# Kernel tuning notes

Measured on AMD Instinct MI355X. Metric: run time of the kernel, lower is better.

Reference implementation:

```python
import jax, jax.numpy as jnp
import numpy as np

N_NODES = 50000
N_EDGES = 800000
D = 64
E_DIM = 16
N_GRAPHS = 5000
BN_EPS = 1e-5


def _xavier(key, shape):
    fan_in, fan_out = shape[0], shape[1]
    limit = np.sqrt(6.0 / (fan_in + fan_out))
    return jax.random.uniform(key, shape, jnp.float32, -limit, limit)


def setup_inputs() -> dict:
    key = jax.random.key(0)
    ks = jax.random.split(key, 16)
    x = jax.random.normal(ks[0], (N_NODES, D), jnp.float32)
    edge_index = jax.random.randint(ks[1], (2, N_EDGES), 0, N_NODES, jnp.int64)
    edge_attr = jax.random.normal(ks[2], (N_EDGES, E_DIM), jnp.float32)
    batch = jnp.sort(jax.random.randint(ks[3], (N_NODES,), 0, N_GRAPHS, jnp.int64))
    zdim = 2 * D + E_DIM  # 144
    params = {
        'fw0': _xavier(ks[4], (zdim, D)), 'fb0': jnp.zeros((D,), jnp.float32),
        'sw0': _xavier(ks[5], (zdim, D)), 'sb0': jnp.zeros((D,), jnp.float32),
        'bng0': jnp.ones((D,), jnp.float32), 'bnb0': jnp.zeros((D,), jnp.float32),
        'fw1': _xavier(ks[6], (zdim, D)), 'fb1': jnp.zeros((D,), jnp.float32),
        'sw1': _xavier(ks[7], (zdim, D)), 'sb1': jnp.zeros((D,), jnp.float32),
        'bng1': jnp.ones((D,), jnp.float32), 'bnb1': jnp.zeros((D,), jnp.float32),
        'pw1': _xavier(ks[8], (D, D)), 'pb1': jnp.zeros((D,), jnp.float32),
        'pw2': _xavier(ks[9], (D, D)), 'pb2': jnp.zeros((D,), jnp.float32),
    }
    return dict(x=x, edge_index=edge_index, edge_attr=edge_attr, batch=batch, **params)


def _cgconv(x, src, dst, e, Wf, bf, Ws, bs):
    # PyG CGConv: x_i' = x_i + sum_j sigmoid(Wf z) * softplus(Ws z), z=[x_i, x_j, e]
    # edge_index[0]=source j, edge_index[1]=target i; aggregate at target.
    z = jnp.concatenate([x[dst], x[src], e], axis=-1)  # [E, 2D+Ed]
    m = jax.nn.sigmoid(z @ Wf + bf) * jax.nn.softplus(z @ Ws + bs)  # [E, D]
    agg = jax.ops.segment_sum(m, dst, num_segments=x.shape[0])
    return x + agg


def _batchnorm(x, gamma, beta):
    mu = jnp.mean(x, axis=0)
    var = jnp.mean(jnp.square(x - mu), axis=0)  # biased, training-mode BN
    return (x - mu) * jax.lax.rsqrt(var + BN_EPS) * gamma + beta


def reference(x, edge_index, edge_attr, batch,
              fw0, fb0, sw0, sb0, bng0, bnb0,
              fw1, fb1, sw1, sb1, bng1, bnb1,
              pw1, pb1, pw2, pb2):
    src, dst = edge_index[0], edge_index[1]
    h = _batchnorm(_cgconv(x, src, dst, edge_attr, fw0, fb0, sw0, sb0), bng0, bnb0)
    h = _batchnorm(_cgconv(h, src, dst, edge_attr, fw1, fb1, sw1, sb1), bng1, bnb1)
    # global mean pool over graphs
    sums = jax.ops.segment_sum(h, batch, num_segments=N_GRAPHS)
    cnt = jax.ops.segment_sum(jnp.ones((h.shape[0],), h.dtype), batch, num_segments=N_GRAPHS)
    pooled = sums / jnp.maximum(cnt, 1.0)[:, None]  # [G, D]
    # proj head: Linear -> LeakyReLU(0.01) -> Linear
    y = jax.nn.leaky_relu(pooled @ pw1 + pb1, negative_slope=0.01)
    return y @ pw2 + pb2
```

## Files before the change

### kernel.cpp

```cpp
#include <hip/hip_runtime.h>

#define NN 50000
#define NE 800000
#define DD 64
#define ED 16
#define NG 5000
#define SS 16

__global__ __launch_bounds__(256) void prep_weights(
    const float* __restrict__ fw0, const float* __restrict__ sw0,
    const float* __restrict__ fw1, const float* __restrict__ sw1,
    float2* __restrict__ Wd0, float2* __restrict__ Wsc0, float2* __restrict__ We0,
    float2* __restrict__ Wd1, float2* __restrict__ Wsc1, float2* __restrict__ We1) {
  int i = blockIdx.x * 256 + threadIdx.x;
  if (i >= 2 * 144 * 64) return;
  int layer = i >= 144 * 64;
  int j = i - layer * 144 * 64;
  int k = j >> 6, d = j & 63;
  const float* fw = layer ? fw1 : fw0;
  const float* sw = layer ? sw1 : sw0;
  float2 v = make_float2(fw[j], sw[j]);
  float2* Wd = layer ? Wd1 : Wd0;
  float2* Wsc = layer ? Wsc1 : Wsc0;
  float2* We = layer ? We1 : We0;
  if (k < 64)       Wd[k * DD + d] = v;
  else if (k < 128) Wsc[(k - 64) * DD + d] = v;
  else              We[(k - 128) * DD + d] = v;
}

__global__ __launch_bounds__(256) void k_hist(const int* __restrict__ ei,
                                              int* __restrict__ deg) {
  int e = blockIdx.x * 256 + threadIdx.x;
  if (e < NE) atomicAdd(&deg[ei[NE + e]], 1);
}

__global__ __launch_bounds__(256) void k_scan1(const int* __restrict__ deg,
                                               int* __restrict__ rowptr,
                                               int* __restrict__ partials) {
  __shared__ int sm[256];
  int t = threadIdx.x, i = blockIdx.x * 256 + t;
  int v = (i < NN) ? deg[i] : 0;
  sm[t] = v; __syncthreads();
  for (int off = 1; off < 256; off <<= 1) {
    int x = (t >= off) ? sm[t - off] : 0;
    __syncthreads();
    sm[t] += x;
    __syncthreads();
  }
  if (i < NN) rowptr[i] = sm[t] - v;
  if (t == 255) partials[blockIdx.x] = sm[255];
}

__global__ __launch_bounds__(256) void k_scan2(int* __restrict__ partials,
                                               int* __restrict__ poff, int nparts) {
  __shared__ int sm[256];
  int t = threadIdx.x;
  int v = (t < nparts) ? partials[t] : 0;
  sm[t] = v; __syncthreads();
  for (int off = 1; off < 256; off <<= 1) {
    int x = (t >= off) ? sm[t - off] : 0;
    __syncthreads();
    sm[t] += x;
    __syncthreads();
  }
  poff[t] = sm[t] - v;
}

__global__ __launch_bounds__(256) void k_scan3(int* __restrict__ rowptr,
                                               int* __restrict__ cursor,
                                               const int* __restrict__ poff) {
  int i = blockIdx.x * 256 + threadIdx.x;
  if (i < NN) {
    int v = rowptr[i] + poff[blockIdx.x];
    rowptr[i] = v;
    cursor[i] = v;
  } else if (i == NN) {
    rowptr[NN] = NE;
  }
}

__global__ __launch_bounds__(256) void k_scatter(const int* __restrict__ ei,
                                                 const float4* __restrict__ ea4,
                                                 int* __restrict__ cursor,
                                                 int* __restrict__ ssrc,
                                                 int* __restrict__ sdst,
                                                 float4* __restrict__ sea4) {
  int e = blockIdx.x * 256 + threadIdx.x;
  if (e >= NE) return;
  int dst = ei[NE + e];
  int pos = atomicAdd(&cursor[dst], 1);
  ssrc[pos] = ei[e];
  sdst[pos] = dst;
  const float4* q = ea4 + (size_t)e * 4;
  float4 a0 = q[0], a1 = q[1], a2 = q[2], a3 = q[3];
  float4* o = sea4 + (size_t)pos * 4;
  o[0] = a0; o[1] = a1; o[2] = a2; o[3] = a3;
}

template <int BN>
__global__ __launch_bounds__(256) void node_transform(
    const float* __restrict__ hin, const float* __restrict__ stats,
    const float* __restrict__ gamma, const float* __restrict__ beta,
    const float2* __restrict__ Wd, const float2* __restrict__ Wsc,
    const float* __restrict__ bf, const float* __restrict__ sbv,
    float2* __restrict__ Dst, float2* __restrict__ Src,
    float* __restrict__ hcopy) {
  __shared__ float hrow[32][DD];
  int tid = threadIdx.x, w = tid >> 6, d = tid & 63;
  int nbase = blockIdx.x * 32;
  const float invN = 1.f / (float)NN;
#pragma unroll
  for (int j = 0; j < 2; ++j) {
    int i4 = tid + j * 256;
    int node = nbase + (i4 >> 4);
    if (node < NN) {
      int c = (i4 & 15) * 4;
      float4 v = *(const float4*)(hin + (size_t)node * DD + c);
      if (BN) {
        float mu0 = stats[c + 0] * invN, va0 = stats[64 + c + 0] * invN - mu0 * mu0;
        float mu1 = stats[c + 1] * invN, va1 = stats[64 + c + 1] * invN - mu1 * mu1;
        float mu2 = stats[c + 2] * invN, va2 = stats[64 + c + 2] * invN - mu2 * mu2;
        float mu3 = stats[c + 3] * invN, va3 = stats[64 + c + 3] * invN - mu3 * mu3;
        float sc0 = rsqrtf(va0 + 1e-5f) * gamma[c + 0];
        float sc1 = rsqrtf(va1 + 1e-5f) * gamma[c + 1];
        float sc2 = rsqrtf(va2 + 1e-5f) * gamma[c + 2];
        float sc3 = rsqrtf(va3 + 1e-5f) * gamma[c + 3];
        v.x = fmaf(v.x, sc0, beta[c + 0] - mu0 * sc0);
        v.y = fmaf(v.y, sc1, beta[c + 1] - mu1 * sc1);
        v.z = fmaf(v.z, sc2, beta[c + 2] - mu2 * sc2);
        v.w = fmaf(v.w, sc3, beta[c + 3] - mu3 * sc3);
      }
      *(float4*)(&hrow[i4 >> 4][c]) = v;
      *(float4*)(hcopy + (size_t)node * DD + c) = v;
    }
  }
  __syncthreads();

  float bfd = bf[d], sbd = sbv[d];
  float2 ad[8], as_[8];
#pragma unroll
  for (int i = 0; i < 8; ++i) { ad[i] = make_float2(bfd, sbd); as_[i] = make_float2(0.f, 0.f); }

  for (int kk = 0; kk < 16; ++kk) {
    int k0 = kk * 4;
    float2 wd0 = Wd[(k0 + 0) * DD + d], wd1 = Wd[(k0 + 1) * DD + d];
    float2 wd2 = Wd[(k0 + 2) * DD + d], wd3 = Wd[(k0 + 3) * DD + d];
    float2 ws0 = Wsc[(k0 + 0) * DD + d], ws1 = Wsc[(k0 + 1) * DD + d];
    float2 ws2 = Wsc[(k0 + 2) * DD + d], ws3 = Wsc[(k0 + 3) * DD + d];
#pragma unroll
    for (int i = 0; i < 8; ++i) {
      float4 hv = *(const float4*)(&hrow[w * 8 + i][k0]);
      ad[i].x = fmaf(hv.x, wd0.x, ad[i].x); ad[i].y = fmaf(hv.x, wd0.y, ad[i].y);
      as_[i].x = fmaf(hv.x, ws0.x, as_[i].x); as_[i].y = fmaf(hv.x, ws0.y, as_[i].y);
      ad[i].x = fmaf(hv.y, wd1.x, ad[i].x); ad[i].y = fmaf(hv.y, wd1.y, ad[i].y);
      as_[i].x = fmaf(hv.y, ws1.x, as_[i].x); as_[i].y = fmaf(hv.y, ws1.y, as_[i].y);
      ad[i].x = fmaf(hv.z, wd2.x, ad[i].x); ad[i].y = fmaf(hv.z, wd2.y, ad[i].y);
      as_[i].x = fmaf(hv.z, ws2.x, as_[i].x); as_[i].y = fmaf(hv.z, ws2.y, as_[i].y);
      ad[i].x = fmaf(hv.w, wd3.x, ad[i].x); ad[i].y = fmaf(hv.w, wd3.y, ad[i].y);
      as_[i].x = fmaf(hv.w, ws3.x, as_[i].x); as_[i].y = fmaf(hv.w, ws3.y, as_[i].y);
    }
  }
#pragma unroll
  for (int i = 0; i < 8; ++i) {
    int n = nbase + w * 8 + i;
    if (n < NN) {
      Dst[(size_t)n * DD + d] = ad[i];
      Src[(size_t)n * DD + d] = as_[i];
    }
  }
}

__global__ __launch_bounds__(256, 4) void conv_strip(
    const int* __restrict__ ssrc, const int* __restrict__ sdst,
    const float4* __restrict__ sea4, const float2* __restrict__ We,
    const float2* __restrict__ Dst, const float2* __restrict__ Src,
    float* __restrict__ out) {
  __shared__ float4 sEA[4][SS * 4];
  __shared__ int sid[4][2 * SS];
  int tid = threadIdx.x, w = tid >> 6, d = tid & 63;
  int strip = blockIdx.x * 4 + w;
  size_t base = (size_t)strip * SS;

  sEA[w][d] = sea4[base * 4 + d];
  if (d < 2 * SS) sid[w][d] = (d < SS) ? ssrc[base + d] : sdst[base + d - SS];
  __syncthreads();

  float2 we[16];
#pragma unroll
  for (int k = 0; k < 16; ++k) we[k] = We[k * DD + d];

  float2 b[SS];
#pragma unroll
  for (int i = 0; i < SS; ++i) b[i] = Src[(size_t)sid[w][i] * DD + d];

  int curdst = sid[w][SS];
  float2 a = Dst[(size_t)curdst * DD + d];
  float acc = 0.f;
#pragma unroll
  for (int i = 0; i < SS; ++i) {
    int dstn = sid[w][SS + i];
    if (dstn != curdst) {
      atomicAdd(&out[(size_t)curdst * DD + d], acc);
      acc = 0.f;
      curdst = dstn;
      a = Dst[(size_t)curdst * DD + d];
    }
    float cf = a.x + b[i].x, cs = a.y + b[i].y;
#pragma unroll
    for (int k = 0; k < 4; ++k) {
      float4 z = sEA[w][i * 4 + k];
      cf = fmaf(z.x, we[4 * k + 0].x, cf); cs = fmaf(z.x, we[4 * k + 0].y, cs);
      cf = fmaf(z.y, we[4 * k + 1].x, cf); cs = fmaf(z.y, we[4 * k + 1].y, cs);
      cf = fmaf(z.z, we[4 * k + 2].x, cf); cs = fmaf(z.z, we[4 * k + 2].y, cs);
      cf = fmaf(z.w, we[4 * k + 3].x, cf); cs = fmaf(z.w, we[4 * k + 3].y, cs);
    }
    float sig = __builtin_amdgcn_rcpf(1.f + __expf(-cf));
    float sp  = fmaxf(cs, 0.f) + __logf(1.f + __expf(-fabsf(cs)));
    acc = fmaf(sig, sp, acc);
  }
  atomicAdd(&out[(size_t)curdst * DD + d], acc);
}

__global__ __launch_bounds__(256) void bn_stats(const float* __restrict__ h,
                                                float* __restrict__ stats) {
  int tid = threadIdx.x;
  int c = (tid & 15) * 4;
  int r0 = blockIdx.x * 16 + (tid >> 4);
  float4 s = make_float4(0, 0, 0, 0), ss = make_float4(0, 0, 0, 0);
  for (int r = r0; r < NN; r += gridDim.x * 16) {
    float4 v = *(const float4*)(h + (size_t)r * DD + c);
    s.x += v.x; s.y += v.y; s.z += v.z; s.w += v.w;
    ss.x += v.x * v.x; ss.y += v.y * v.y; ss.z += v.z * v.z; ss.w += v.w * v.w;
  }
  __shared__ float4 sm[256], sm2[256];
  sm[tid] = s; sm2[tid] = ss;
  __syncthreads();
  for (int str = 128; str >= 16; str >>= 1) {
    if (tid < str) {
      sm[tid].x += sm[tid + str].x; sm[tid].y += sm[tid + str].y;
      sm[tid].z += sm[tid + str].z; sm[tid].w += sm[tid + str].w;
      sm2[tid].x += sm2[tid + str].x; sm2[tid].y += sm2[tid + str].y;
      sm2[tid].z += sm2[tid + str].z; sm2[tid].w += sm2[tid + str].w;
    }
    __syncthreads();
  }
  if (tid < 16) {
    int cc = tid * 4;
    atomicAdd(&stats[cc + 0], sm[tid].x); atomicAdd(&stats[cc + 1], sm[tid].y);
    atomicAdd(&stats[cc + 2], sm[tid].z); atomicAdd(&stats[cc + 3], sm[tid].w);
    atomicAdd(&stats[64 + cc + 0], sm2[tid].x); atomicAdd(&stats[64 + cc + 1], sm2[tid].y);
    atomicAdd(&stats[64 + cc + 2], sm2[tid].z); atomicAdd(&stats[64 + cc + 3], sm2[tid].w);
  }
}

__global__ __launch_bounds__(256) void pool_bn(
    const float* __restrict__ h, const int* __restrict__ batch,
    const float* __restrict__ stats,
    const float* __restrict__ gamma, const float* __restrict__ beta,
    float* __restrict__ psum, float* __restrict__ pcnt) {
  int tid = threadIdx.x, g = tid >> 6, d = tid & 63;
  const float invN = 1.f / (float)NN;
  float mu = stats[d] * invN;
  float var = stats[64 + d] * invN - mu * mu;
  float sc = rsqrtf(var + 1e-5f) * gamma[d];
  float sh = beta[d] - mu * sc;
  int n0 = (blockIdx.x * 4 + g) * 32;
  if (n0 >= NN) return;
  int nend = n0 + 32; if (nend > NN) nend = NN;
  int bprev = batch[n0];
  float acc = 0.f; int run = 0;
  for (int n = n0; n < nend; ++n) {
    int b = batch[n];
    if (b != bprev) {
      atomicAdd(&psum[(size_t)bprev * DD + d], acc);
      if (d == 0) atomicAdd(&pcnt[bprev], (float)run);
      acc = 0.f; run = 0; bprev = b;
    }
    acc += fmaf(h[(size_t)n * DD + d], sc, sh);
    ++run;
  }
  atomicAdd(&psum[(size_t)bprev * DD + d], acc);
  if (d == 0) atomicAdd(&pcnt[bprev], (float)run);
}

__global__ __launch_bounds__(256) void head_kernel(
    const float* __restrict__ psum, const float* __restrict__ pcnt,
    const float* __restrict__ pw1, const float* __restrict__ pb1,
    const float* __restrict__ pw2, const float* __restrict__ pb2,
    float* __restrict__ out) {
  __shared__ float row[4][DD], y1[4][DD];
  int tid = threadIdx.x, g = tid >> 6, d = tid & 63;
  int q = blockIdx.x * 4 + g;
  float c = fmaxf(pcnt[q], 1.0f);
  row[g][d] = psum[(size_t)q * DD + d] * __builtin_amdgcn_rcpf(c);
  __syncthreads();
  float acc = pb1[d];
#pragma unroll
  for (int k = 0; k < DD; ++k) acc = fmaf(row[g][k], pw1[k * DD + d], acc);
  acc = acc > 0.f ? acc : 0.01f * acc;
  y1[g][d] = acc;
  __syncthreads();
  float o = pb2[d];
#pragma unroll
  for (int k = 0; k < DD; ++k) o = fmaf(y1[g][k], pw2[k * DD + d], o);
  out[(size_t)q * DD + d] = o;
}

extern "C" void kernel_launch(void* const* d_in, const int* in_sizes, int n_in,
                              void* d_out, int out_size, void* d_ws, size_t ws_size,
                              hipStream_t stream) {
  const float* x     = (const float*)d_in[0];
  const int*   ei    = (const int*)d_in[1];
  const float* ea    = (const float*)d_in[2];
  const int*   batch = (const int*)d_in[3];
  const float* fw0 = (const float*)d_in[4],  *fb0 = (const float*)d_in[5];
  const float* sw0 = (const float*)d_in[6],  *sb0 = (const float*)d_in[7];
  const float* bng0= (const float*)d_in[8],  *bnb0= (const float*)d_in[9];
  const float* fw1 = (const float*)d_in[10], *fb1 = (const float*)d_in[11];
  const float* sw1 = (const float*)d_in[12], *sb1 = (const float*)d_in[13];
  const float* bng1= (const float*)d_in[14], *bnb1= (const float*)d_in[15];
  const float* pw1 = (const float*)d_in[16], *pb1 = (const float*)d_in[17];
  const float* pw2 = (const float*)d_in[18], *pb2 = (const float*)d_in[19];

  const size_t NND = (size_t)NN * DD;
  float4* sea4 = (float4*)d_ws;
  float2* Wd0  = (float2*)(sea4 + (size_t)NE * 4);
  float2* Wsc0 = Wd0 + 64 * DD;
  float2* We0  = Wsc0 + 64 * DD;
  float2* Wd1  = We0 + ED * DD;
  float2* Wsc1 = Wd1 + 64 * DD;
  float2* We1  = Wsc1 + 64 * DD;
  float2* Dst  = We1 + ED * DD;
  float2* Src  = Dst + NND;
  float*  h1   = (float*)(Src + NND);
  float*  h2   = h1 + NND;
  int*    deg    = (int*)(h2 + NND);
  float*  stats0 = (float*)(deg + NN);
  float*  stats1 = stats0 + 256;
  float*  psum   = stats1 + 256;
  float*  pcnt   = psum + (size_t)NG * DD;
  int* rowptr   = (int*)(pcnt + NG);
  int* cursor   = rowptr + NN + 1;
  int* partials = cursor + NN;
  int* poff     = partials + 256;
  int* ssrc     = poff + 256;
  int* sdst     = ssrc + NE;

  const int NB_NODE = (NN + 255) / 256;

  hipMemsetAsync(deg, 0,
                 ((size_t)NN + 512 + (size_t)NG * DD + NG) * sizeof(float), stream);
  prep_weights<<<72, 256, 0, stream>>>(fw0, sw0, fw1, sw1,
                                       Wd0, Wsc0, We0, Wd1, Wsc1, We1);

  k_hist<<<(NE + 255) / 256, 256, 0, stream>>>(ei, deg);
  k_scan1<<<NB_NODE, 256, 0, stream>>>(deg, rowptr, partials);
  k_scan2<<<1, 256, 0, stream>>>(partials, poff, NB_NODE);
  k_scan3<<<(NN + 256) / 256, 256, 0, stream>>>(rowptr, cursor, poff);
  k_scatter<<<(NE + 255) / 256, 256, 0, stream>>>(ei, (const float4*)ea, cursor,
                                                  ssrc, sdst, sea4);

  node_transform<0><<<(NN + 31) / 32, 256, 0, stream>>>(
      x, nullptr, nullptr, nullptr, Wd0, Wsc0, fb0, sb0, Dst, Src, h1);
  conv_strip<<<NE / SS / 4, 256, 0, stream>>>(ssrc, sdst, sea4, We0, Dst, Src, h1);
  bn_stats<<<128, 256, 0, stream>>>(h1, stats0);

  node_transform<1><<<(NN + 31) / 32, 256, 0, stream>>>(
      h1, stats0, bng0, bnb0, Wd1, Wsc1, fb1, sb1, Dst, Src, h2);
  conv_strip<<<NE / SS / 4, 256, 0, stream>>>(ssrc, sdst, sea4, We1, Dst, Src, h2);
  bn_stats<<<128, 256, 0, stream>>>(h2, stats1);

  pool_bn<<<391, 256, 0, stream>>>(h2, batch, stats1, bng1, bnb1, psum, pcnt);
  head_kernel<<<NG / 4, 256, 0, stream>>>(psum, pcnt, pw1, pb1, pw2, pb2, (float*)d_out);
}
```

Baseline: 570.6 us.

## Double-buffer source gathers in conv strip with longer strips and 32-bit addressing

Doubles the edges per wave strip to 32. Instead of loading all source rows up front, the kernel now loads them in groups of four with a double buffer, which cuts register use and raises the occupancy hint to 6. Address math moves to 32-bit byte offsets. Longer strips mean fewer atomics at segment boundaries, but each block has less parallelism and any prefetch overlap depends on the compiler.

```diff
diff --git a/kernel.cpp b/kernel.cpp
--- a/kernel.cpp
+++ b/kernel.cpp
@@ -5,7 +5,7 @@
 #define DD 64
 #define ED 16
 #define NG 5000
-#define SS 16
+#define SS 32
 
 __global__ __launch_bounds__(256) void prep_weights(
     const float* __restrict__ fw0, const float* __restrict__ sw0,
@@ -170,7 +170,7 @@
   }
 }
 
-__global__ __launch_bounds__(256, 4) void conv_strip(
+__global__ __launch_bounds__(256, 6) void conv_strip(
     const int* __restrict__ ssrc, const int* __restrict__ sdst,
     const float4* __restrict__ sea4, const float2* __restrict__ We,
     const float2* __restrict__ Dst, const float2* __restrict__ Src,
@@ -179,46 +179,68 @@
   __shared__ int sid[4][2 * SS];
   int tid = threadIdx.x, w = tid >> 6, d = tid & 63;
   int strip = blockIdx.x * 4 + w;
-  size_t base = (size_t)strip * SS;
-
-  sEA[w][d] = sea4[base * 4 + d];
-  if (d < 2 * SS) sid[w][d] = (d < SS) ? ssrc[base + d] : sdst[base + d - SS];
+  int base = strip * SS;
+
+  sEA[w][d]      = sea4[(size_t)base * 4 + d];
+  sEA[w][64 + d] = sea4[(size_t)base * 4 + 64 + d];
+  sid[w][d] = (d < SS) ? ssrc[base + d] : sdst[base + (d - SS)];
   __syncthreads();
 
   float2 we[16];
 #pragma unroll
   for (int k = 0; k < 16; ++k) we[k] = We[k * DD + d];
 
-  float2 b[SS];
-#pragma unroll
-  for (int i = 0; i < SS; ++i) b[i] = Src[(size_t)sid[w][i] * DD + d];
+  const char* SrcB = (const char*)Src;
+  const char* DstB = (const char*)Dst;
+  unsigned doff = (unsigned)d * 8u;
+
+#define LOADSRC(n) (*(const float2*)(SrcB + (((unsigned)(n)) << 9) + doff))
+#define LOADDST(n) (*(const float2*)(DstB + (((unsigned)(n)) << 9) + doff))
+
+  float2 bufA[4], bufB[4];
+#pragma unroll
+  for (int j = 0; j < 4; ++j) bufA[j] = LOADSRC(sid[w][j]);
 
   int curdst = sid[w][SS];
-  float2 a = Dst[(size_t)curdst * DD + d];
+  float2 a = LOADDST(curdst);
   float acc = 0.f;
-#pragma unroll
-  for (int i = 0; i < SS; ++i) {
-    int dstn = sid[w][SS + i];
-    if (dstn != curdst) {
-      atomicAdd(&out[(size_t)curdst * DD + d], acc);
-      acc = 0.f;
-      curdst = dstn;
-      a = Dst[(size_t)curdst * DD + d];
-    }
-    float cf = a.x + b[i].x, cs = a.y + b[i].y;
-#pragma unroll
-    for (int k = 0; k < 4; ++k) {
-      float4 z = sEA[w][i * 4 + k];
-      cf = fmaf(z.x, we[4 * k + 0].x, cf); cs = fmaf(z.x, we[4 * k + 0].y, cs);
-      cf = fmaf(z.y, we[4 * k + 1].x, cf); cs = fmaf(z.y, we[4 * k + 1].y, cs);
-      cf = fmaf(z.z, we[4 * k + 2].x, cf); cs = fmaf(z.z, we[4 * k + 2].y, cs);
-      cf = fmaf(z.w, we[4 * k + 3].x, cf); cs = fmaf(z.w, we[4 * k + 3].y, cs);
-    }
-    float sig = __builtin_amdgcn_rcpf(1.f + __expf(-cf));
-    float sp  = fmaxf(cs, 0.f) + __logf(1.f + __expf(-fabsf(cs)));
-    acc = fmaf(sig, sp, acc);
-  }
-  atomicAdd(&out[(size_t)curdst * DD + d], acc);
+
+#pragma unroll
+  for (int g = 0; g < SS / 4; ++g) {
+    float2* cur = (g & 1) ? bufB : bufA;
+    float2* nxt = (g & 1) ? bufA : bufB;
+    if (g < SS / 4 - 1) {
+#pragma unroll
+      for (int j = 0; j < 4; ++j) nxt[j] = LOADSRC(sid[w][g * 4 + 4 + j]);
+    }
+#pragma unroll
+    for (int j = 0; j < 4; ++j) {
+      int i = g * 4 + j;
+      int dstn = sid[w][SS + i];
+      if (dstn != curdst) {
+        atomicAdd(&out[(unsigned)curdst * 64u + (unsigned)d], acc);
+        acc = 0.f;
+        curdst = dstn;
+        a = LOADDST(curdst);
+      }
+      float2 b = cur[j];
+      float cf = a.x + b.x, cs = a.y + b.y;
+#pragma unroll
+      for (int k = 0; k < 4; ++k) {
+        float4 z = sEA[w][i * 4 + k];
+        cf = fmaf(z.x, we[4 * k + 0].x, cf); cs = fmaf(z.x, we[4 * k + 0].y, cs);
+        cf = fmaf(z.y, we[4 * k + 1].x, cf); cs = fmaf(z.y, we[4 * k + 1].y, cs);
+        cf = fmaf(z.z, we[4 * k + 2].x, cf); cs = fmaf(z.z, we[4 * k + 2].y, cs);
+        cf = fmaf(z.w, we[4 * k + 3].x, cf); cs = fmaf(z.w, we[4 * k + 3].y, cs);
+      }
+      float sig = __builtin_amdgcn_rcpf(1.f + __expf(-cf));
+      float sp  = fmaxf(cs, 0.f) + __logf(1.f + __expf(-fabsf(cs)));
+      acc = fmaf(sig, sp, acc);
+    }
+  }
+  atomicAdd(&out[(unsigned)curdst * 64u + (unsigned)d], acc);
+#undef LOADSRC
+#undef LOADDST
 }
 
 __global__ __launch_bounds__(256) void bn_stats(const float* __restrict__ h,
```

Result: no change. 578.5 us (+1.4%).
